# Kernel tuning notes

Hardware: AMD Instinct MI355X
Metric: run time of the kernel (lower is better)

## Reference

```python
import jax, jax.numpy as jnp
import numpy as np

N = 50000      # nodes
E = 800000     # edges (avg degree 16)
IN = 128       # in_ft
OUT = 128      # out_ft
T = 2          # num_types (hard-coded by F.one_hot(num_classes=2))


def setup_inputs() -> dict:
    key = jax.random.key(0)
    ks = jax.random.split(key, 10)
    gain = 1.414
    seq = jax.random.normal(ks[0], (N, IN), jnp.float32)
    edge_weight = jax.random.uniform(ks[1], (E,), jnp.float32)
    edge_row = jax.random.randint(ks[2], (E,), 0, N, jnp.int32)   # receivers (spmm output rows)
    edge_col = jax.random.randint(ks[3], (E,), 0, N, jnp.int32)   # senders
    node_type = jax.random.randint(ks[4], (N,), 0, T, jnp.int32)
    # xavier_normal with gain 1.414, stored as [in, out] so x @ W matches nn.Linear
    W_fc = jax.random.normal(ks[5], (IN, OUT), jnp.float32) * (gain * np.sqrt(2.0 / (IN + OUT)))
    W_gamma = jax.random.normal(ks[6], (T, OUT), jnp.float32) * (gain * np.sqrt(2.0 / (T + OUT)))
    W_beta = jax.random.normal(ks[7], (T, OUT), jnp.float32) * (gain * np.sqrt(2.0 / (T + OUT)))
    b_gamma = jnp.zeros((OUT,), jnp.float32)
    b_beta = jnp.zeros((OUT,), jnp.float32)
    bias = jnp.zeros((OUT,), jnp.float32)
    prelu_w = jnp.full((1,), 0.25, jnp.float32)  # nn.PReLU default: single shared slope 0.25
    return {"seq": seq, "edge_weight": edge_weight, "W_fc": W_fc,
            "W_gamma": W_gamma, "b_gamma": b_gamma, "W_beta": W_beta, "b_beta": b_beta,
            "bias": bias, "prelu_w": prelu_w,
            "edge_row": edge_row, "edge_col": edge_col, "node_type": node_type}


def reference(seq, edge_weight, W_fc, W_gamma, b_gamma, W_beta, b_beta, bias, prelu_w,
              edge_row, edge_col, node_type):
    # seq_fts = fc(seq)
    seq_fts = seq @ W_fc                                   # [N, OUT]
    # out = spmm(adj, seq_fts): gather sender feats, scale by edge weight, sum into receivers
    msg = edge_weight[:, None] * seq_fts[edge_col]         # [E, OUT]
    out = jax.ops.segment_sum(msg, edge_row, num_segments=N)  # [N, OUT]
    # FiLM: gamma/beta from one-hot node type (== row select of W + bias)
    one_hot = jax.nn.one_hot(node_type, T, dtype=seq.dtype)   # [N, 2]
    gamma = one_hot @ W_gamma + b_gamma                    # [N, OUT]
    beta = one_hot @ W_beta + b_beta                       # [N, OUT]
    out = gamma * out + beta + bias + seq_fts              # FiLM + bias + residual
    # PReLU with single shared slope
    return jnp.where(out >= 0, out, prelu_w[0] * out)
```

## Files before the change

### kernel.cpp

```cpp
#include <hip/hip_runtime.h>

#define IN_F 128
#define OUT_F 128
#define BKLOG 5
#define BKN 32
#define CAP 1024
#define SLOTS 56
#define CHUNK 4096
#define SCT 512

typedef __attribute__((ext_vector_type(8))) short short8v;
typedef __attribute__((ext_vector_type(4))) float float4v;

static __device__ __forceinline__ unsigned f2bf(float x) {
    unsigned b = __float_as_uint(x);
    return (b + 0x7FFFu + ((b >> 16) & 1u)) >> 16;
}
static __device__ __forceinline__ float bfLo(unsigned u) { return __uint_as_float(u << 16); }
static __device__ __forceinline__ float bfHi(unsigned u) { return __uint_as_float(u & 0xFFFF0000u); }

static __device__ __forceinline__ void edge_fma(float ww, uint4 vv, float* a) {
    a[0] = fmaf(ww, bfLo(vv.x), a[0]); a[1] = fmaf(ww, bfHi(vv.x), a[1]);
    a[2] = fmaf(ww, bfLo(vv.y), a[2]); a[3] = fmaf(ww, bfHi(vv.y), a[3]);
    a[4] = fmaf(ww, bfLo(vv.z), a[4]); a[5] = fmaf(ww, bfHi(vv.z), a[5]);
    a[6] = fmaf(ww, bfLo(vv.w), a[6]); a[7] = fmaf(ww, bfHi(vv.w), a[7]);
}

__global__ __launch_bounds__(256) void prep_kernel(const float* __restrict__ W,
                                                   unsigned short* __restrict__ Wt,
                                                   int* __restrict__ gcur, int NBK)
{
    const int b = blockIdx.x;
    if (b < 64) {
        int i = b * 256 + threadIdx.x;
        int k = i >> 7, c = i & 127;
        Wt[c * 128 + k] = (unsigned short)f2bf(W[i]);
    } else {
        for (int i = threadIdx.x; i <= NBK; i += 256) gcur[i] = 0;
    }
}

__global__ __launch_bounds__(256) void gemm_mfma(
    const float* __restrict__ A, const unsigned short* __restrict__ Wt,
    unsigned short* __restrict__ Cb, int nrows)
{
    __shared__ unsigned short Al[64][136];
    __shared__ unsigned short Wl[128][136];
    const int t = threadIdx.x;
    const int rowBase = blockIdx.x * 64;

#pragma unroll
    for (int i = 0; i < 8; ++i) {
        int q  = t + i * 256;
        int c  = q >> 4;
        int kb = (q & 15) * 8;
        *(uint4*)(&Wl[c][kb]) = *(const uint4*)(Wt + c * 128 + kb);
    }
#pragma unroll
    for (int i = 0; i < 8; ++i) {
        int q  = t + i * 256;
        int r  = q >> 5;
        int k4 = (q & 31) * 4;
        int gr = rowBase + r;
        if (gr >= nrows) gr = nrows - 1;
        float4 v = *(const float4*)(A + (size_t)gr * IN_F + k4);
        uint2 pk;
        pk.x = f2bf(v.x) | (f2bf(v.y) << 16);
        pk.y = f2bf(v.z) | (f2bf(v.w) << 16);
        *(uint2*)(&Al[r][k4]) = pk;
    }
    __syncthreads();

    const int w    = t >> 6;
    const int lane = t & 63;
    const int rb   = w * 16;
    const int m    = lane & 15;
    const int kg   = (lane >> 4) * 8;

    float4v acc[8];
#pragma unroll
    for (int n = 0; n < 8; ++n) acc[n] = (float4v){0.f, 0.f, 0.f, 0.f};

#pragma unroll
    for (int ks = 0; ks < 4; ++ks) {
        short8v a = *(const short8v*)(&Al[rb + m][ks * 32 + kg]);
#pragma unroll
        for (int n = 0; n < 8; ++n) {
            short8v bf = *(const short8v*)(&Wl[n * 16 + m][ks * 32 + kg]);
            acc[n] = __builtin_amdgcn_mfma_f32_16x16x32_bf16(a, bf, acc[n], 0, 0, 0);
        }
    }

    const int orow = rowBase + rb + (lane >> 4) * 4;
#pragma unroll
    for (int n = 0; n < 8; ++n) {
#pragma unroll
        for (int j = 0; j < 4; ++j) {
            int r = orow + j;
            if (r < nrows)
                Cb[(size_t)r * OUT_F + n * 16 + m] = (unsigned short)f2bf(acc[n][j]);
        }
    }
}

__global__ __launch_bounds__(SCT) void scatter_fix(
    const int* __restrict__ row, const int* __restrict__ col,
    const float* __restrict__ ew, int* __restrict__ gcur,
    uint2* __restrict__ bucket, uint2* __restrict__ ovf, int E, int NBK)
{
    __shared__ int h[2048];
    const int t = threadIdx.x;
    const int base = blockIdx.x * CHUNK;
    const int lim  = min(CHUNK, E - base);

    for (int i = t; i < 2048; i += SCT) h[i] = 0;
    __syncthreads();

    int   rc[8]; float wc[8]; int cc[8];
#pragma unroll
    for (int k = 0; k < 8; ++k) {
        int i = t + k * SCT;
        if (i < lim) {
            rc[k] = row[base + i];
            wc[k] = ew[base + i];
            cc[k] = col[base + i];
            atomicAdd(&h[rc[k] >> BKLOG], 1);
        } else rc[k] = -1;
    }
    __syncthreads();

    for (int i = t; i < NBK; i += SCT) {
        int c = h[i];
        if (c) h[i] = atomicAdd(&gcur[i], c);
    }
    __syncthreads();

#pragma unroll
    for (int k = 0; k < 8; ++k) {
        if (rc[k] >= 0) {
            int r = rc[k];
            int b = r >> BKLOG;
            int p = atomicAdd(&h[b], 1);
            uint2 rec;
            rec.x = __float_as_uint(wc[k]);
            if (p < CAP) {
                rec.y = ((unsigned)(r & (BKN - 1)) << 16) | (unsigned)cc[k];
                bucket[(size_t)b * CAP + p] = rec;
            } else {
                int q = atomicAdd(&gcur[NBK], 1);
                rec.y = ((unsigned)r << 16) | (unsigned)cc[k];
                ovf[q] = rec;
            }
        }
    }
}

__global__ __launch_bounds__(256) void spmm64_film(
    const int* __restrict__ gcur, const uint2* __restrict__ bucket,
    const uint2* __restrict__ ovf,
    const unsigned short* __restrict__ seqb, const int* __restrict__ ntype,
    const float* __restrict__ Wg, const float* __restrict__ bg,
    const float* __restrict__ Wb, const float* __restrict__ bb,
    const float* __restrict__ bias, const float* __restrict__ prelu,
    float* __restrict__ out, int N, int NBK)
{
    __shared__ uint2 slot[BKN * SLOTS];
    __shared__ int   bc[BKN];

    const int t = threadIdx.x;
    const int b = blockIdx.x;
    const uint2* breg = bucket + (size_t)b * CAP;
    const int total = gcur[b];
    const int inb   = min(total, CAP);

    if (t < BKN) bc[t] = 0;
    __syncthreads();

    for (int i = t; i < inb; i += 256) {
        uint2 rec = breg[i];
        int n = (rec.y >> 16) & (BKN - 1);
        int pos = atomicAdd(&bc[n], 1);
        if (pos < SLOTS) slot[n * SLOTS + pos] = rec;
    }
    __syncthreads();

    const int l  = t & 15;
    const int f0 = l * 8;
    const float sl = prelu[0];

    for (int g = 0; g < 2; ++g) {
        const int nl = g * 16 + (t >> 4);
        const int node = (b << BKLOG) + nl;
        if (node >= N) continue;

        const int deg = bc[nl];
        float a[8] = {0.f, 0.f, 0.f, 0.f, 0.f, 0.f, 0.f, 0.f};

        if (deg <= SLOTS) {
            const uint2* sp = &slot[nl * SLOTS];
            int j = 0;
            for (; j + 2 <= deg; j += 2) {
                uint2 r0 = sp[j], r1 = sp[j + 1];
                float w0 = __uint_as_float(r0.x);
                float w1 = __uint_as_float(r1.x);
                const uint4 v0 = *(const uint4*)(seqb + ((size_t)(r0.y & 0xFFFFu) << 7) + f0);
                const uint4 v1 = *(const uint4*)(seqb + ((size_t)(r1.y & 0xFFFFu) << 7) + f0);
                edge_fma(w0, v0, a);
                edge_fma(w1, v1, a);
            }
            if (j < deg) {
                uint2 r0 = sp[j];
                float w0 = __uint_as_float(r0.x);
                const uint4 v0 = *(const uint4*)(seqb + ((size_t)(r0.y & 0xFFFFu) << 7) + f0);
                edge_fma(w0, v0, a);
            }
        } else {
            for (int i = 0; i < inb; ++i) {
                uint2 rec = breg[i];
                if ((int)((rec.y >> 16) & (BKN - 1)) == nl) {
                    float w = __uint_as_float(rec.x);
                    const uint4 v = *(const uint4*)(seqb + ((size_t)(rec.y & 0xFFFFu) << 7) + f0);
                    edge_fma(w, v, a);
                }
            }
        }
        if (total > CAP) {
            const int novf = gcur[NBK];
            for (int i = 0; i < novf; ++i) {
                uint2 rec = ovf[i];
                if ((int)(rec.y >> 16) == node) {
                    float w = __uint_as_float(rec.x);
                    const uint4 v = *(const uint4*)(seqb + ((size_t)(rec.y & 0xFFFFu) << 7) + f0);
                    edge_fma(w, v, a);
                }
            }
        }

        const int tp = ntype[node];
        float4 g0 = *(const float4*)(Wg + tp * OUT_F + f0);
        float4 g1 = *(const float4*)(Wg + tp * OUT_F + f0 + 4);
        float4 h0 = *(const float4*)(bg + f0);
        float4 h1 = *(const float4*)(bg + f0 + 4);
        float4 p0 = *(const float4*)(Wb + tp * OUT_F + f0);
        float4 p1 = *(const float4*)(Wb + tp * OUT_F + f0 + 4);
        float4 q0 = *(const float4*)(bb + f0);
        float4 q1 = *(const float4*)(bb + f0 + 4);
        float4 s0 = *(const float4*)(bias + f0);
        float4 s1 = *(const float4*)(bias + f0 + 4);
        uint4  rs = *(const uint4*)(seqb + ((size_t)node << 7) + f0);

        float gg[8] = {g0.x + h0.x, g0.y + h0.y, g0.z + h0.z, g0.w + h0.w,
                       g1.x + h1.x, g1.y + h1.y, g1.z + h1.z, g1.w + h1.w};
        float pb[8] = {p0.x + q0.x + s0.x, p0.y + q0.y + s0.y, p0.z + q0.z + s0.z, p0.w + q0.w + s0.w,
                       p1.x + q1.x + s1.x, p1.y + q1.y + s1.y, p1.z + q1.z + s1.z, p1.w + q1.w + s1.w};
        float rv[8] = {bfLo(rs.x), bfHi(rs.x), bfLo(rs.y), bfHi(rs.y),
                       bfLo(rs.z), bfHi(rs.z), bfLo(rs.w), bfHi(rs.w)};
        float oo[8];
#pragma unroll
        for (int k = 0; k < 8; ++k) {
            float v = fmaf(gg[k], a[k], pb[k]) + rv[k];
            oo[k] = (v >= 0.f) ? v : sl * v;
        }
        *(float4*)(out + ((size_t)node << 7) + f0)     = make_float4(oo[0], oo[1], oo[2], oo[3]);
        *(float4*)(out + ((size_t)node << 7) + f0 + 4) = make_float4(oo[4], oo[5], oo[6], oo[7]);
    }
}

extern "C" void kernel_launch(void* const* d_in, const int* in_sizes, int n_in,
                              void* d_out, int out_size, void* d_ws, size_t ws_size,
                              hipStream_t stream)
{
    const float* seq   = (const float*)d_in[0];
    const float* ew    = (const float*)d_in[1];
    const float* W_fc  = (const float*)d_in[2];
    const float* W_g   = (const float*)d_in[3];
    const float* b_g   = (const float*)d_in[4];
    const float* W_b   = (const float*)d_in[5];
    const float* b_b   = (const float*)d_in[6];
    const float* bias  = (const float*)d_in[7];
    const float* prelu = (const float*)d_in[8];
    const int*   erow  = (const int*)d_in[9];
    const int*   ecol  = (const int*)d_in[10];
    const int*   ntype = (const int*)d_in[11];
    const int N = in_sizes[11];
    const int E = in_sizes[1];
    const int NBK = (N + BKN - 1) >> BKLOG;
    const int NCH = (E + CHUNK - 1) / CHUNK;

    char* ws = (char*)d_ws;
    size_t o = 0;
    unsigned short* seqb = (unsigned short*)(ws + o); o += (size_t)N * OUT_F * 2; o = (o + 15) & ~(size_t)15;
    unsigned short* Wt   = (unsigned short*)(ws + o); o += (size_t)IN_F * OUT_F * 2;
    int*   gcur = (int*)(ws + o);  o += 2049 * 4 + 12; o &= ~(size_t)15;
    uint2* bucket = (uint2*)(ws + o); o += (size_t)NBK * CAP * 8;
    uint2* ovf    = (uint2*)(ws + o); o += (size_t)E * 8;

    hipLaunchKernelGGL(prep_kernel, dim3(65), dim3(256), 0, stream, W_fc, Wt, gcur, NBK);
    hipLaunchKernelGGL(scatter_fix, dim3(NCH), dim3(SCT), 0, stream,
                       erow, ecol, ew, gcur, bucket, ovf, E, NBK);
    hipLaunchKernelGGL(gemm_mfma, dim3((N + 63) / 64), dim3(256), 0, stream, seq, Wt, seqb, N);
    hipLaunchKernelGGL(spmm64_film, dim3(NBK), dim3(256), 0, stream,
                       gcur, bucket, ovf, seqb, ntype, W_g, b_g, W_b, b_b, bias, prelu,
                       (float*)d_out, N, NBK);
}
```

Before: 70.01 us.

## Fuse edge bucketing scatter and bf16 GEMM into one heterogeneous kernel launch

Merges the edge-bucketing scatter kernel and the MFMA GEMM into a single launch: the first NCH blocks do the scatter and the remaining blocks each compute 128 rows of the projection with 512 threads, sharing one raw LDS buffer. This removes a kernel launch and the serialization between two independent stages, so scatter and GEMM can run concurrently on the GPU. The larger GEMM tile doubles LDS use per block (about 70 KB), which may lower occupancy for both roles.

```diff
diff --git a/kernel.cpp b/kernel.cpp
--- a/kernel.cpp
+++ b/kernel.cpp
@@ -40,116 +40,118 @@
     }
 }
 
-__global__ __launch_bounds__(256) void gemm_mfma(
+__global__ __launch_bounds__(SCT) void fused_sg(
+    const int* __restrict__ row, const int* __restrict__ col,
+    const float* __restrict__ ew, int* __restrict__ gcur,
+    uint2* __restrict__ bucket, uint2* __restrict__ ovf, int E, int NBK, int NCH,
     const float* __restrict__ A, const unsigned short* __restrict__ Wt,
     unsigned short* __restrict__ Cb, int nrows)
 {
-    __shared__ unsigned short Al[64][136];
-    __shared__ unsigned short Wl[128][136];
+    __shared__ __align__(16) char ldsraw[2 * 128 * 136 * 2];
+
     const int t = threadIdx.x;
-    const int rowBase = blockIdx.x * 64;
-
-#pragma unroll
-    for (int i = 0; i < 8; ++i) {
-        int q  = t + i * 256;
-        int c  = q >> 4;
-        int kb = (q & 15) * 8;
-        *(uint4*)(&Wl[c][kb]) = *(const uint4*)(Wt + c * 128 + kb);
-    }
-#pragma unroll
-    for (int i = 0; i < 8; ++i) {
-        int q  = t + i * 256;
-        int r  = q >> 5;
-        int k4 = (q & 31) * 4;
-        int gr = rowBase + r;
-        if (gr >= nrows) gr = nrows - 1;
-        float4 v = *(const float4*)(A + (size_t)gr * IN_F + k4);
-        uint2 pk;
-        pk.x = f2bf(v.x) | (f2bf(v.y) << 16);
-        pk.y = f2bf(v.z) | (f2bf(v.w) << 16);
-        *(uint2*)(&Al[r][k4]) = pk;
-    }
-    __syncthreads();
-
-    const int w    = t >> 6;
-    const int lane = t & 63;
-    const int rb   = w * 16;
-    const int m    = lane & 15;
-    const int kg   = (lane >> 4) * 8;
-
-    float4v acc[8];
-#pragma unroll
-    for (int n = 0; n < 8; ++n) acc[n] = (float4v){0.f, 0.f, 0.f, 0.f};
-
-#pragma unroll
-    for (int ks = 0; ks < 4; ++ks) {
-        short8v a = *(const short8v*)(&Al[rb + m][ks * 32 + kg]);
+
+    if (blockIdx.x < (unsigned)NCH) {
+        int* h = (int*)ldsraw;
+        const int base = blockIdx.x * CHUNK;
+        const int lim  = min(CHUNK, E - base);
+
+        for (int i = t; i < 2048; i += SCT) h[i] = 0;
+        __syncthreads();
+
+        int   rc[8]; float wc[8]; int cc[8];
+#pragma unroll
+        for (int k = 0; k < 8; ++k) {
+            int i = t + k * SCT;
+            if (i < lim) {
+                rc[k] = row[base + i];
+                wc[k] = ew[base + i];
+                cc[k] = col[base + i];
+                atomicAdd(&h[rc[k] >> BKLOG], 1);
+            } else rc[k] = -1;
+        }
+        __syncthreads();
+
+        for (int i = t; i < NBK; i += SCT) {
+            int c = h[i];
+            if (c) h[i] = atomicAdd(&gcur[i], c);
+        }
+        __syncthreads();
+
+#pragma unroll
+        for (int k = 0; k < 8; ++k) {
+            if (rc[k] >= 0) {
+                int r = rc[k];
+                int b = r >> BKLOG;
+                int p = atomicAdd(&h[b], 1);
+                uint2 rec;
+                rec.x = __float_as_uint(wc[k]);
+                if (p < CAP) {
+                    rec.y = ((unsigned)(r & (BKN - 1)) << 16) | (unsigned)cc[k];
+                    bucket[(size_t)b * CAP + p] = rec;
+                } else {
+                    int q = atomicAdd(&gcur[NBK], 1);
+                    rec.y = ((unsigned)r << 16) | (unsigned)cc[k];
+                    ovf[q] = rec;
+                }
+            }
+        }
+    } else {
+        typedef unsigned short ushort136[136];
+        ushort136* Al = (ushort136*)ldsraw;
+        ushort136* Wl = (ushort136*)(ldsraw + 128 * 136 * 2);
+        const int rowBase = (blockIdx.x - NCH) * 128;
+
+#pragma unroll
+        for (int i = 0; i < 4; ++i) {
+            int q  = t + i * SCT;
+            int c  = q >> 4;
+            int kb = (q & 15) * 8;
+            *(uint4*)(&Wl[c][kb]) = *(const uint4*)(Wt + c * 128 + kb);
+        }
+#pragma unroll
+        for (int i = 0; i < 8; ++i) {
+            int q  = t + i * SCT;
+            int r  = q >> 5;
+            int k4 = (q & 31) * 4;
+            int gr = rowBase + r;
+            if (gr >= nrows) gr = nrows - 1;
+            float4 v = *(const float4*)(A + (size_t)gr * IN_F + k4);
+            uint2 pk;
+            pk.x = f2bf(v.x) | (f2bf(v.y) << 16);
+            pk.y = f2bf(v.z) | (f2bf(v.w) << 16);
+            *(uint2*)(&Al[r][k4]) = pk;
+        }
+        __syncthreads();
+
+        const int w    = t >> 6;
+        const int lane = t & 63;
+        const int rb   = w * 16;
+        const int m    = lane & 15;
+        const int kg   = (lane >> 4) * 8;
+
+        float4v acc[8];
+#pragma unroll
+        for (int n = 0; n < 8; ++n) acc[n] = (float4v){0.f, 0.f, 0.f, 0.f};
+
+#pragma unroll
+        for (int ks = 0; ks < 4; ++ks) {
+            short8v a = *(const short8v*)(&Al[rb + m][ks * 32 + kg]);
+#pragma unroll
+            for (int n = 0; n < 8; ++n) {
+                short8v bf = *(const short8v*)(&Wl[n * 16 + m][ks * 32 + kg]);
+                acc[n] = __builtin_amdgcn_mfma_f32_16x16x32_bf16(a, bf, acc[n], 0, 0, 0);
+            }
+        }
+
+        const int orow = rowBase + rb + (lane >> 4) * 4;
 #pragma unroll
         for (int n = 0; n < 8; ++n) {
-            short8v bf = *(const short8v*)(&Wl[n * 16 + m][ks * 32 + kg]);
-            acc[n] = __builtin_amdgcn_mfma_f32_16x16x32_bf16(a, bf, acc[n], 0, 0, 0);
-        }
-    }
-
-    const int orow = rowBase + rb + (lane >> 4) * 4;
-#pragma unroll
-    for (int n = 0; n < 8; ++n) {
-#pragma unroll
-        for (int j = 0; j < 4; ++j) {
-            int r = orow + j;
-            if (r < nrows)
-                Cb[(size_t)r * OUT_F + n * 16 + m] = (unsigned short)f2bf(acc[n][j]);
-        }
-    }
-}
-
-__global__ __launch_bounds__(SCT) void scatter_fix(
-    const int* __restrict__ row, const int* __restrict__ col,
-    const float* __restrict__ ew, int* __restrict__ gcur,
-    uint2* __restrict__ bucket, uint2* __restrict__ ovf, int E, int NBK)
-{
-    __shared__ int h[2048];
-    const int t = threadIdx.x;
-    const int base = blockIdx.x * CHUNK;
-    const int lim  = min(CHUNK, E - base);
-
-    for (int i = t; i < 2048; i += SCT) h[i] = 0;
-    __syncthreads();
-
-    int   rc[8]; float wc[8]; int cc[8];
-#pragma unroll
-    for (int k = 0; k < 8; ++k) {
-        int i = t + k * SCT;
-        if (i < lim) {
-            rc[k] = row[base + i];
-            wc[k] = ew[base + i];
-            cc[k] = col[base + i];
-            atomicAdd(&h[rc[k] >> BKLOG], 1);
-        } else rc[k] = -1;
-    }
-    __syncthreads();
-
-    for (int i = t; i < NBK; i += SCT) {
-        int c = h[i];
-        if (c) h[i] = atomicAdd(&gcur[i], c);
-    }
-    __syncthreads();
-
-#pragma unroll
-    for (int k = 0; k < 8; ++k) {
-        if (rc[k] >= 0) {
-            int r = rc[k];
-            int b = r >> BKLOG;
-            int p = atomicAdd(&h[b], 1);
-            uint2 rec;
-            rec.x = __float_as_uint(wc[k]);
-            if (p < CAP) {
-                rec.y = ((unsigned)(r & (BKN - 1)) << 16) | (unsigned)cc[k];
-                bucket[(size_t)b * CAP + p] = rec;
-            } else {
-                int q = atomicAdd(&gcur[NBK], 1);
-                rec.y = ((unsigned)r << 16) | (unsigned)cc[k];
-                ovf[q] = rec;
+#pragma unroll
+            for (int j = 0; j < 4; ++j) {
+                int r = orow + j;
+                if (r < nrows)
+                    Cb[(size_t)r * OUT_F + n * 16 + m] = (unsigned short)f2bf(acc[n][j]);
             }
         }
     }
@@ -286,6 +288,7 @@
     const int E = in_sizes[1];
     const int NBK = (N + BKN - 1) >> BKLOG;
     const int NCH = (E + CHUNK - 1) / CHUNK;
+    const int GB  = (N + 127) / 128;
 
     char* ws = (char*)d_ws;
     size_t o = 0;
@@ -296,9 +299,9 @@
     uint2* ovf    = (uint2*)(ws + o); o += (size_t)E * 8;
 
     hipLaunchKernelGGL(prep_kernel, dim3(65), dim3(256), 0, stream, W_fc, Wt, gcur, NBK);
-    hipLaunchKernelGGL(scatter_fix, dim3(NCH), dim3(SCT), 0, stream,
-                       erow, ecol, ew, gcur, bucket, ovf, E, NBK);
-    hipLaunchKernelGGL(gemm_mfma, dim3((N + 63) / 64), dim3(256), 0, stream, seq, Wt, seqb, N);
+    hipLaunchKernelGGL(fused_sg, dim3(NCH + GB), dim3(SCT), 0, stream,
+                       erow, ecol, ew, gcur, bucket, ovf, E, NBK, NCH,
+                       seq, Wt, seqb, N);
     hipLaunchKernelGGL(spmm64_film, dim3(NBK), dim3(256), 0, stream,
                        gcur, bucket, ovf, seqb, ntype, W_g, b_g, W_b, b_b, bias, prelu,
                        (float*)d_out, N, NBK);
```

After: 64.86 us (median of 2 runs). 7.4% less time.
